# Kernel optimization log

Hardware: AMD Instinct MI355X
Metric: run time of the kernel (lower is better)

Reference implementation:

```python
import jax, jax.numpy as jnp
import numpy as np

T, B, D = 1024, 4, 1024  # seq_len, batch, d_model (module is seq-first: data[T,B,D])


def setup_inputs() -> dict:
    key = jax.random.key(0)
    ks = jax.random.split(key, 5)
    data = jax.random.normal(ks[0], (T, B, D), jnp.float32)
    # torch Linear equivalent: y = x @ W + b with W stored [in, out]
    W_qkv = jax.random.normal(ks[1], (D, 3 * D), jnp.float32) * 0.02
    b_qkv = jnp.zeros((3 * D,), jnp.float32)
    # Pos_bias param interpolated to [T,T]; with T == seq_len it's the raw param.
    pos_bias = jax.random.normal(ks[2], (T, T), jnp.float32) * 0.02
    W_out = jax.random.normal(ks[3], (D, D), jnp.float32) * 0.02
    b_out = jnp.zeros((D,), jnp.float32)
    return dict(data=data, W_qkv=W_qkv, b_qkv=b_qkv, pos_bias=pos_bias,
                W_out=W_out, b_out=b_out)


def reference(data, W_qkv, b_qkv, pos_bias, W_out, b_out):
    # layer_norm=False -> Identity; dropout unused in forward
    qkv = data @ W_qkv + b_qkv                 # [T,B,3D]
    q, k, v = jnp.split(qkv, 3, axis=-1)       # each [T,B,D]
    P = jnp.exp(pos_bias)                      # [T,T], exp of (identity-interpolated) pos bias
    ek = jnp.exp(k)                            # [T,B,D]
    # einsum 'ijb,jbd->ibd' with b==1 broadcast on pos_bias == 'tj,jbd->tbd'
    num = jnp.einsum('tj,jbd->tbd', P, ek * v)  # [T,B,D]
    den = jnp.einsum('tj,jbd->tbd', P, ek)      # [T,B,D]
    out = jax.nn.sigmoid(q) * (num / den)       # gated AFT output
    return out @ W_out + b_out                  # [T,B,D]
```

## Files before the change

kernel.cpp:

```cpp
#include <hip/hip_runtime.h>
#include <hip/hip_bf16.h>
#include <cstdint>
#include <cstddef>


typedef __bf16 bf16_t;
typedef __attribute__((ext_vector_type(8))) __bf16 bf16x8;
typedef __attribute__((ext_vector_type(4))) __bf16 bf16x4;
typedef __attribute__((ext_vector_type(4))) float floatx4;

#define T_DIM 1024
#define B_DIM 4
#define D_DIM 1024
#define R_DIM (T_DIM * B_DIM)
#define N_QKV (3 * D_DIM)
#define N_ND  (2 * R_DIM)

__global__ void k_prep(const float* __restrict__ data, const float* __restrict__ pos_bias,
                       const float* __restrict__ W_qkv, const float* __restrict__ W_out,
                       bf16_t* __restrict__ data_bf, bf16_t* __restrict__ P_bf,
                       bf16_t* __restrict__ WqT, bf16_t* __restrict__ WkvTi,
                       bf16_t* __restrict__ WoutT) {
    __shared__ float s[32][33];
    const int bid = blockIdx.x, tid = threadIdx.x;
    if (bid < 5120) {
        const float* in = (bid < 4096) ? data : pos_bias;
        bf16_t* out = (bid < 4096) ? data_bf : P_bf;
        int bb = (bid < 4096) ? bid : bid - 4096;
        int do_exp = (bid >= 4096);
        int i = (bb * 256 + tid) * 4;
        float4 v = *reinterpret_cast<const float4*>(in + i);
        bf16x4 o;
        if (do_exp) {
            o[0] = (bf16_t)__expf(v.x); o[1] = (bf16_t)__expf(v.y);
            o[2] = (bf16_t)__expf(v.z); o[3] = (bf16_t)__expf(v.w);
        } else {
            o[0] = (bf16_t)v.x; o[1] = (bf16_t)v.y;
            o[2] = (bf16_t)v.z; o[3] = (bf16_t)v.w;
        }
        *reinterpret_cast<bf16x4*>(out + i) = o;
    } else if (bid < 8192) {
        int idx = bid - 5120;
        int n0 = (idx % 96) * 32, k0 = (idx / 96) * 32;
        int tx = tid & 31, ty = tid >> 5;
#pragma unroll
        for (int i = 0; i < 4; ++i)
            s[ty + i * 8][tx] = W_qkv[(size_t)(k0 + ty + i * 8) * N_QKV + n0 + tx];
        __syncthreads();
#pragma unroll
        for (int i = 0; i < 4; ++i) {
            int n = n0 + ty + i * 8;
            bf16_t val = (bf16_t)s[tx][ty + i * 8];
            bf16_t* dst; size_t row;
            if (n < 1024)      { dst = WqT;   row = n; }
            else if (n < 2048) { int d = n - 1024; dst = WkvTi; row = ((d >> 4) << 5) + (d & 15); }
            else               { int d = n - 2048; dst = WkvTi; row = ((d >> 4) << 5) + (d & 15) + 16; }
            dst[row * D_DIM + k0 + tx] = val;
        }
    } else {
        int idx = bid - 8192;
        int n0 = (idx % 32) * 32, k0 = (idx / 32) * 32;
        int tx = tid & 31, ty = tid >> 5;
#pragma unroll
        for (int i = 0; i < 4; ++i)
            s[ty + i * 8][tx] = W_out[(size_t)(k0 + ty + i * 8) * D_DIM + n0 + tx];
        __syncthreads();
#pragma unroll
        for (int i = 0; i < 4; ++i)
            WoutT[(size_t)(n0 + ty + i * 8) * D_DIM + k0 + tx] = (bf16_t)s[tx][ty + i * 8];
    }
}

__device__ __forceinline__ void gload16(const bf16_t* src, bf16_t* dst) {
    __builtin_amdgcn_global_load_lds(
        (const __attribute__((address_space(1))) void*)src,
        (__attribute__((address_space(3))) void*)dst, 16, 0, 0);
}

__device__ __forceinline__ void mfma_loop(
    const bf16_t* __restrict__ aSrc0, const bf16_t* __restrict__ aSrc1,
    const bf16_t* __restrict__ bSrc0, const bf16_t* __restrict__ bSrc1,
    bf16_t* As, bf16_t* Bs, int wid, int lane, int K, floatx4 (&acc)[4][4]) {
    const int lr = lane & 15, kq = (lane >> 4) * 8;
    const int wm = wid >> 1, wn = wid & 1;
    for (int kt = 0; kt < K; kt += 32) {
        __syncthreads();
        gload16(aSrc0 + kt, As + wid * 1024);
        gload16(aSrc1 + kt, As + wid * 1024 + 512);
        gload16(bSrc0 + kt, Bs + wid * 1024);
        gload16(bSrc1 + kt, Bs + wid * 1024 + 512);
        __syncthreads();
        bf16x8 af[4], bfr[4];
#pragma unroll
        for (int m = 0; m < 4; ++m)
            af[m] = *reinterpret_cast<const bf16x8*>(As + (wm * 64 + m * 16 + lr) * 32 + kq);
#pragma unroll
        for (int n = 0; n < 4; ++n)
            bfr[n] = *reinterpret_cast<const bf16x8*>(Bs + (wn * 64 + n * 16 + lr) * 32 + kq);
#pragma unroll
        for (int m = 0; m < 4; ++m)
#pragma unroll
            for (int n = 0; n < 4; ++n)
                acc[m][n] = __builtin_amdgcn_mfma_f32_16x16x32_bf16(af[m], bfr[n], acc[m][n], 0, 0, 0);
    }
}

#define GEMM_PREAMBLE(K)                                              \
    __shared__ __align__(16) bf16_t As[128 * 32];                     \
    __shared__ __align__(16) bf16_t Bs[128 * 32];                     \
    const int tid = threadIdx.x;                                      \
    const int wid = tid >> 6, lane = tid & 63;                        \
    const int wm = wid >> 1, wn = wid & 1;                            \
    floatx4 acc[4][4];                                                \
    _Pragma("unroll") for (int m = 0; m < 4; ++m)                     \
        _Pragma("unroll") for (int n = 0; n < 4; ++n)                 \
            acc[m][n] = (floatx4){0.f, 0.f, 0.f, 0.f};                \
    const int lr = lane & 15;                                         \
    const int e0 = wid * 1024 + lane * 8;                             \
    const int ra0 = e0 >> 5, kk0 = e0 & 31;                           \
    const int ra1 = (e0 + 512) >> 5, kk1 = (e0 + 512) & 31;           \
    const int lg = lane >> 4; (void)lg; (void)K;

__global__ __launch_bounds__(256)
void k_gemm(const bf16_t* __restrict__ A, const bf16_t* __restrict__ BT,
            const float* __restrict__ bias, float* __restrict__ C,
            int M, int N, int K) {
    GEMM_PREAMBLE(K)
    const int row0 = blockIdx.x * 128, col0 = blockIdx.y * 128;
    mfma_loop(A + (size_t)(row0 + ra0) * K + kk0, A + (size_t)(row0 + ra1) * K + kk1,
              BT + (size_t)(col0 + ra0) * K + kk0, BT + (size_t)(col0 + ra1) * K + kk1,
              As, Bs, wid, lane, K, acc);
#pragma unroll
    for (int n = 0; n < 4; ++n) {
        int col = col0 + wn * 64 + n * 16 + lr;
        float bv = bias ? bias[col] : 0.0f;
#pragma unroll
        for (int m = 0; m < 4; ++m) {
            int row = row0 + wm * 64 + m * 16 + lg * 4;
            float* Cp = C + (size_t)row * N + col;
#pragma unroll
            for (int j = 0; j < 4; ++j) Cp[(size_t)j * N] = acc[m][n][j] + bv;
        }
    }
}

__global__ __launch_bounds__(256)
void k_gemm_qkv(const bf16_t* __restrict__ data_bf, const bf16_t* __restrict__ WqT,
                const bf16_t* __restrict__ WkvTi, const float* __restrict__ b_qkv,
                float* __restrict__ q_buf, bf16_t* __restrict__ BndT) {
    const int K = D_DIM;
    GEMM_PREAMBLE(K)
    const int bid = blockIdx.x;
    if (bid < 256) {
        const int row0 = (bid >> 3) * 128, col0 = (bid & 7) * 128;
        mfma_loop(data_bf + (size_t)(row0 + ra0) * K + kk0,
                  data_bf + (size_t)(row0 + ra1) * K + kk1,
                  WqT + (size_t)(col0 + ra0) * K + kk0,
                  WqT + (size_t)(col0 + ra1) * K + kk1,
                  As, Bs, wid, lane, K, acc);
#pragma unroll
        for (int n = 0; n < 4; ++n) {
            int col = col0 + wn * 64 + n * 16 + lr;
            float bv = b_qkv[col];
#pragma unroll
            for (int m = 0; m < 4; ++m) {
                int row = row0 + wm * 64 + m * 16 + lg * 4;
                float* Cp = q_buf + (size_t)row * D_DIM + col;
#pragma unroll
                for (int j = 0; j < 4; ++j) Cp[(size_t)j * D_DIM] = acc[m][n][j] + bv;
            }
        }
    } else {
        const int idx = bid - 256;
        const int b = idx >> 7;
        const int row0 = ((idx & 127) >> 3) * 128;
        const int col0 = (idx & 7) * 128;
        mfma_loop(WkvTi + (size_t)(row0 + ra0) * K + kk0,
                  WkvTi + (size_t)(row0 + ra1) * K + kk1,
                  data_bf + ((size_t)(col0 + ra0) * 4 + b) * D_DIM + kk0,
                  data_bf + ((size_t)(col0 + ra1) * 4 + b) * D_DIM + kk1,
                  As, Bs, wid, lane, K, acc);
#pragma unroll
        for (int p = 0; p < 2; ++p) {
#pragma unroll
            for (int j = 0; j < 4; ++j) {
                int gk = row0 + wm * 64 + p * 32 + lg * 4 + j;
                int d = ((gk >> 5) << 4) + (lg * 4 + j);
                float bk = b_qkv[D_DIM + d];
                float bv = b_qkv[2 * D_DIM + d];
                int r = b * D_DIM + d;
                int rr = ((r >> 4) << 5) + (r & 15);
#pragma unroll
                for (int n = 0; n < 4; ++n) {
                    int t = col0 + wn * 64 + n * 16 + lr;
                    float e = __expf(acc[2 * p][n][j] + bk);
                    float vv = acc[2 * p + 1][n][j] + bv;
                    BndT[(size_t)rr * T_DIM + t] = (bf16_t)(e * vv);
                    BndT[(size_t)(rr + 16) * T_DIM + t] = (bf16_t)e;
                }
            }
        }
    }
}

__global__ __launch_bounds__(256)
void k_gemm_aft(const bf16_t* __restrict__ A, const bf16_t* __restrict__ BT,
                const float* __restrict__ q, bf16_t* __restrict__ Y) {
    const int K = T_DIM;
    GEMM_PREAMBLE(K)
    const int row0 = blockIdx.x * 128, col0 = blockIdx.y * 128;
    mfma_loop(A + (size_t)(row0 + ra0) * K + kk0, A + (size_t)(row0 + ra1) * K + kk1,
              BT + (size_t)(col0 + ra0) * K + kk0, BT + (size_t)(col0 + ra1) * K + kk1,
              As, Bs, wid, lane, K, acc);
#pragma unroll
    for (int p = 0; p < 2; ++p) {
        int ncol = col0 + wn * 64 + p * 32 + lr;
        int r = ((ncol >> 5) << 4) + lr;
#pragma unroll
        for (int m = 0; m < 4; ++m) {
            int trow = row0 + wm * 64 + m * 16 + lg * 4;
#pragma unroll
            for (int j = 0; j < 4; ++j) {
                int t = trow + j;
                float num = acc[m][2 * p][j];
                float den = acc[m][2 * p + 1][j];
                float qv = q[(size_t)t * R_DIM + r];
                float y = num / (den * (1.0f + __expf(-qv)));
                Y[(size_t)t * R_DIM + r] = (bf16_t)y;
            }
        }
    }
}

extern "C" void kernel_launch(void* const* d_in, const int* in_sizes, int n_in,
                              void* d_out, int out_size, void* d_ws, size_t ws_size,
                              hipStream_t stream) {
    const float* data     = (const float*)d_in[0];
    const float* W_qkv    = (const float*)d_in[1];
    const float* b_qkv    = (const float*)d_in[2];
    const float* pos_bias = (const float*)d_in[3];
    const float* W_out    = (const float*)d_in[4];
    const float* b_out    = (const float*)d_in[5];
    float* out = (float*)d_out;

    char* ws = (char*)d_ws;
    const size_t MB = 1024 * 1024;
    bf16_t* data_bf = (bf16_t*)(ws + 0);
    bf16_t* WqT     = (bf16_t*)(ws + 8 * MB);
    bf16_t* WkvTi   = (bf16_t*)(ws + 10 * MB);
    bf16_t* WoutT   = (bf16_t*)(ws + 14 * MB);
    bf16_t* P_bf    = (bf16_t*)(ws + 16 * MB);
    float*  q_buf   = (float*) (ws + 18 * MB);
    bf16_t* BndT    = (bf16_t*)(ws + 34 * MB);
    bf16_t* Y       = (bf16_t*)(ws + 0);

    k_prep<<<dim3(9216), dim3(256), 0, stream>>>(data, pos_bias, W_qkv, W_out,
                                                 data_bf, P_bf, WqT, WkvTi, WoutT);
    k_gemm_qkv<<<dim3(768), dim3(256), 0, stream>>>(data_bf, WqT, WkvTi, b_qkv,
                                                    q_buf, BndT);
    k_gemm_aft<<<dim3(T_DIM / 128, N_ND / 128), dim3(256), 0, stream>>>(
        P_bf, BndT, q_buf, Y);
    k_gemm<<<dim3(R_DIM / 128, D_DIM / 128), dim3(256), 0, stream>>>(
        Y, WoutT, b_out, out, R_DIM, D_DIM, D_DIM);
}
```

Before: 178.2 us.

## Use 256x256 double-buffered tiles for QKV and AFT GEMMs

Replaces the 128x128 single-buffered QKV and AFT GEMM kernels with 256x256 tile kernels. Each uses 512 threads in 8 waves with an 8x4 MFMA fragment block per wave, and double-buffers LDS so the next K-slice loads while the current one computes. MFMA sections are wrapped in s_setprio. The larger tiles raise operand reuse and cut barrier stalls, but shrink the grids to 192 and 128 blocks, which may underfill the 256 CUs, and raise register pressure.

```diff
diff --git a/kernel.cpp b/kernel.cpp
--- a/kernel.cpp
+++ b/kernel.cpp
@@ -77,6 +77,146 @@
         (__attribute__((address_space(3))) void*)dst, 16, 0, 0);
 }
 
+__device__ __forceinline__ void stage32(const bf16_t* A0, int sA,
+                                        const bf16_t* B0, int sB, int k0,
+                                        bf16_t* AsB, bf16_t* BsB, int wid, int lane) {
+    const int r0 = wid * 16 + (lane >> 2);
+    const int c = (lane & 3) * 8;
+#pragma unroll
+    for (int j = 0; j < 2; ++j) {
+        gload16(A0 + (size_t)(r0 + j * 128) * sA + k0 + c, AsB + j * 4096 + wid * 512);
+        gload16(B0 + (size_t)(r0 + j * 128) * sB + k0 + c, BsB + j * 4096 + wid * 512);
+    }
+}
+
+__device__ __forceinline__ void tile32(const bf16_t* As, const bf16_t* Bs,
+                                       int wm, int wn, int lane, floatx4 (&acc)[8][4]) {
+    const int lr = lane & 15, k0 = (lane >> 4) * 8;
+    bf16x8 a[8], b[4];
+#pragma unroll
+    for (int mf = 0; mf < 8; ++mf)
+        a[mf] = *reinterpret_cast<const bf16x8*>(As + (wm * 128 + mf * 16 + lr) * 32 + k0);
+#pragma unroll
+    for (int nf = 0; nf < 4; ++nf)
+        b[nf] = *reinterpret_cast<const bf16x8*>(Bs + (wn * 64 + nf * 16 + lr) * 32 + k0);
+    __builtin_amdgcn_s_setprio(1);
+#pragma unroll
+    for (int mf = 0; mf < 8; ++mf)
+#pragma unroll
+        for (int nf = 0; nf < 4; ++nf)
+            acc[mf][nf] = __builtin_amdgcn_mfma_f32_16x16x32_bf16(a[mf], b[nf], acc[mf][nf], 0, 0, 0);
+    __builtin_amdgcn_s_setprio(0);
+}
+
+#define PRE256()                                                      \
+    __shared__ __align__(16) bf16_t As0[256 * 32], Bs0[256 * 32];     \
+    __shared__ __align__(16) bf16_t As1[256 * 32], Bs1[256 * 32];     \
+    const int tid = threadIdx.x;                                      \
+    const int wid = tid >> 6, lane = tid & 63;                        \
+    const int wm = wid >> 2, wn = wid & 3;                            \
+    const int lr = lane & 15, lg = lane >> 4;                         \
+    floatx4 acc[8][4];                                                \
+    _Pragma("unroll") for (int mf = 0; mf < 8; ++mf)                  \
+        _Pragma("unroll") for (int nf = 0; nf < 4; ++nf)              \
+            acc[mf][nf] = (floatx4){0.f, 0.f, 0.f, 0.f};
+
+#define LOOP256(Ab, sA, Bb, sB)                                       \
+    stage32(Ab, sA, Bb, sB, 0, As0, Bs0, wid, lane);                  \
+    __syncthreads();                                                  \
+    for (int t2 = 0; t2 < 16; ++t2) {                                 \
+        stage32(Ab, sA, Bb, sB, t2 * 64 + 32, As1, Bs1, wid, lane);   \
+        tile32(As0, Bs0, wm, wn, lane, acc);                          \
+        __syncthreads();                                              \
+        if (t2 < 15)                                                  \
+            stage32(Ab, sA, Bb, sB, t2 * 64 + 64, As0, Bs0, wid, lane);\
+        tile32(As1, Bs1, wm, wn, lane, acc);                          \
+        __syncthreads();                                              \
+    }
+
+__global__ __launch_bounds__(512, 1)
+void k_qkv256(const bf16_t* __restrict__ data_bf, const bf16_t* __restrict__ WqT,
+              const bf16_t* __restrict__ WkvTi, const float* __restrict__ b_qkv,
+              float* __restrict__ q_buf, bf16_t* __restrict__ BndT) {
+    PRE256()
+    const int bid = blockIdx.x;
+    if (bid < 64) {
+        const int row0 = (bid >> 2) * 256, col0 = (bid & 3) * 256;
+        const bf16_t* Ab = data_bf + (size_t)row0 * D_DIM;
+        const bf16_t* Bb = WqT + (size_t)col0 * D_DIM;
+        LOOP256(Ab, D_DIM, Bb, D_DIM)
+#pragma unroll
+        for (int nf = 0; nf < 4; ++nf) {
+            int col = col0 + wn * 64 + nf * 16 + lr;
+            float bv = b_qkv[col];
+#pragma unroll
+            for (int mf = 0; mf < 8; ++mf) {
+                int row = row0 + wm * 128 + mf * 16 + lg * 4;
+                float* Cp = q_buf + (size_t)row * D_DIM + col;
+#pragma unroll
+                for (int j = 0; j < 4; ++j) Cp[(size_t)j * D_DIM] = acc[mf][nf][j] + bv;
+            }
+        }
+    } else {
+        const int idx = bid - 64;
+        const int b = idx >> 5;
+        const int row0 = ((idx & 31) >> 2) * 256;
+        const int col0 = (idx & 3) * 256;
+        const bf16_t* Ab = WkvTi + (size_t)row0 * D_DIM;
+        const bf16_t* Bb = data_bf + ((size_t)col0 * 4 + b) * D_DIM;
+        LOOP256(Ab, D_DIM, Bb, 4 * D_DIM)
+#pragma unroll
+        for (int p = 0; p < 4; ++p) {
+#pragma unroll
+            for (int j = 0; j < 4; ++j) {
+                int gk = row0 + wm * 128 + p * 32 + lg * 4 + j;
+                int d = ((gk >> 5) << 4) + (lg * 4 + j);
+                float bk = b_qkv[D_DIM + d];
+                float bvv = b_qkv[2 * D_DIM + d];
+                int r = b * D_DIM + d;
+                int rr = ((r >> 4) << 5) + (r & 15);
+#pragma unroll
+                for (int nf = 0; nf < 4; ++nf) {
+                    int t = col0 + wn * 64 + nf * 16 + lr;
+                    float e = __expf(acc[2 * p][nf][j] + bk);
+                    float vv = acc[2 * p + 1][nf][j] + bvv;
+                    BndT[(size_t)rr * T_DIM + t] = (bf16_t)(e * vv);
+                    BndT[(size_t)(rr + 16) * T_DIM + t] = (bf16_t)e;
+                }
+            }
+        }
+    }
+}
+
+__global__ __launch_bounds__(512, 1)
+void k_aft256(const bf16_t* __restrict__ P_bf, const bf16_t* __restrict__ BndT,
+              const float* __restrict__ q, bf16_t* __restrict__ Y) {
+    PRE256()
+    const int bid = blockIdx.x;
+    const int row0 = (bid >> 5) * 256;
+    const int col0 = (bid & 31) * 256;
+    const bf16_t* Ab = P_bf + (size_t)row0 * T_DIM;
+    const bf16_t* Bb = BndT + (size_t)col0 * T_DIM;
+    LOOP256(Ab, T_DIM, Bb, T_DIM)
+#pragma unroll
+    for (int p = 0; p < 2; ++p) {
+        int ncol = col0 + wn * 64 + p * 32 + lr;
+        int r = ((ncol >> 5) << 4) + lr;
+#pragma unroll
+        for (int mf = 0; mf < 8; ++mf) {
+            int trow = row0 + wm * 128 + mf * 16 + lg * 4;
+#pragma unroll
+            for (int j = 0; j < 4; ++j) {
+                int t = trow + j;
+                float num = acc[mf][2 * p][j];
+                float den = acc[mf][2 * p + 1][j];
+                float qv = q[(size_t)t * R_DIM + r];
+                float y = num / (den * (1.0f + __expf(-qv)));
+                Y[(size_t)t * R_DIM + r] = (bf16_t)y;
+            }
+        }
+    }
+}
+
 __device__ __forceinline__ void mfma_loop(
     const bf16_t* __restrict__ aSrc0, const bf16_t* __restrict__ aSrc1,
     const bf16_t* __restrict__ bSrc0, const bf16_t* __restrict__ bSrc1,
@@ -105,27 +245,25 @@
     }
 }
 
-#define GEMM_PREAMBLE(K)                                              \
-    __shared__ __align__(16) bf16_t As[128 * 32];                     \
-    __shared__ __align__(16) bf16_t Bs[128 * 32];                     \
-    const int tid = threadIdx.x;                                      \
-    const int wid = tid >> 6, lane = tid & 63;                        \
-    const int wm = wid >> 1, wn = wid & 1;                            \
-    floatx4 acc[4][4];                                                \
-    _Pragma("unroll") for (int m = 0; m < 4; ++m)                     \
-        _Pragma("unroll") for (int n = 0; n < 4; ++n)                 \
-            acc[m][n] = (floatx4){0.f, 0.f, 0.f, 0.f};                \
-    const int lr = lane & 15;                                         \
-    const int e0 = wid * 1024 + lane * 8;                             \
-    const int ra0 = e0 >> 5, kk0 = e0 & 31;                           \
-    const int ra1 = (e0 + 512) >> 5, kk1 = (e0 + 512) & 31;           \
-    const int lg = lane >> 4; (void)lg; (void)K;
-
 __global__ __launch_bounds__(256)
 void k_gemm(const bf16_t* __restrict__ A, const bf16_t* __restrict__ BT,
             const float* __restrict__ bias, float* __restrict__ C,
             int M, int N, int K) {
-    GEMM_PREAMBLE(K)
+    __shared__ __align__(16) bf16_t As[128 * 32];
+    __shared__ __align__(16) bf16_t Bs[128 * 32];
+    const int tid = threadIdx.x;
+    const int wid = tid >> 6, lane = tid & 63;
+    const int wm = wid >> 1, wn = wid & 1;
+    floatx4 acc[4][4];
+#pragma unroll
+    for (int m = 0; m < 4; ++m)
+#pragma unroll
+        for (int n = 0; n < 4; ++n) acc[m][n] = (floatx4){0.f, 0.f, 0.f, 0.f};
+    const int lr = lane & 15;
+    const int e0 = wid * 1024 + lane * 8;
+    const int ra0 = e0 >> 5, kk0 = e0 & 31;
+    const int ra1 = (e0 + 512) >> 5, kk1 = (e0 + 512) & 31;
+    const int lg = lane >> 4;
     const int row0 = blockIdx.x * 128, col0 = blockIdx.y * 128;
     mfma_loop(A + (size_t)(row0 + ra0) * K + kk0, A + (size_t)(row0 + ra1) * K + kk1,
               BT + (size_t)(col0 + ra0) * K + kk0, BT + (size_t)(col0 + ra1) * K + kk1,
@@ -140,94 +278,6 @@
             float* Cp = C + (size_t)row * N + col;
 #pragma unroll
             for (int j = 0; j < 4; ++j) Cp[(size_t)j * N] = acc[m][n][j] + bv;
-        }
-    }
-}
-
-__global__ __launch_bounds__(256)
-void k_gemm_qkv(const bf16_t* __restrict__ data_bf, const bf16_t* __restrict__ WqT,
-                const bf16_t* __restrict__ WkvTi, const float* __restrict__ b_qkv,
-                float* __restrict__ q_buf, bf16_t* __restrict__ BndT) {
-    const int K = D_DIM;
-    GEMM_PREAMBLE(K)
-    const int bid = blockIdx.x;
-    if (bid < 256) {
-        const int row0 = (bid >> 3) * 128, col0 = (bid & 7) * 128;
-        mfma_loop(data_bf + (size_t)(row0 + ra0) * K + kk0,
-                  data_bf + (size_t)(row0 + ra1) * K + kk1,
-                  WqT + (size_t)(col0 + ra0) * K + kk0,
-                  WqT + (size_t)(col0 + ra1) * K + kk1,
-                  As, Bs, wid, lane, K, acc);
-#pragma unroll
-        for (int n = 0; n < 4; ++n) {
-            int col = col0 + wn * 64 + n * 16 + lr;
-            float bv = b_qkv[col];
-#pragma unroll
-            for (int m = 0; m < 4; ++m) {
-                int row = row0 + wm * 64 + m * 16 + lg * 4;
-                float* Cp = q_buf + (size_t)row * D_DIM + col;
-#pragma unroll
-                for (int j = 0; j < 4; ++j) Cp[(size_t)j * D_DIM] = acc[m][n][j] + bv;
-            }
-        }
-    } else {
-        const int idx = bid - 256;
-        const int b = idx >> 7;
-        const int row0 = ((idx & 127) >> 3) * 128;
-        const int col0 = (idx & 7) * 128;
-        mfma_loop(WkvTi + (size_t)(row0 + ra0) * K + kk0,
-                  WkvTi + (size_t)(row0 + ra1) * K + kk1,
-                  data_bf + ((size_t)(col0 + ra0) * 4 + b) * D_DIM + kk0,
-                  data_bf + ((size_t)(col0 + ra1) * 4 + b) * D_DIM + kk1,
-                  As, Bs, wid, lane, K, acc);
-#pragma unroll
-        for (int p = 0; p < 2; ++p) {
-#pragma unroll
-            for (int j = 0; j < 4; ++j) {
-                int gk = row0 + wm * 64 + p * 32 + lg * 4 + j;
-                int d = ((gk >> 5) << 4) + (lg * 4 + j);
-                float bk = b_qkv[D_DIM + d];
-                float bv = b_qkv[2 * D_DIM + d];
-                int r = b * D_DIM + d;
-                int rr = ((r >> 4) << 5) + (r & 15);
-#pragma unroll
-                for (int n = 0; n < 4; ++n) {
-                    int t = col0 + wn * 64 + n * 16 + lr;
-                    float e = __expf(acc[2 * p][n][j] + bk);
-                    float vv = acc[2 * p + 1][n][j] + bv;
-                    BndT[(size_t)rr * T_DIM + t] = (bf16_t)(e * vv);
-                    BndT[(size_t)(rr + 16) * T_DIM + t] = (bf16_t)e;
-                }
-            }
-        }
-    }
-}
-
-__global__ __launch_bounds__(256)
-void k_gemm_aft(const bf16_t* __restrict__ A, const bf16_t* __restrict__ BT,
-                const float* __restrict__ q, bf16_t* __restrict__ Y) {
-    const int K = T_DIM;
-    GEMM_PREAMBLE(K)
-    const int row0 = blockIdx.x * 128, col0 = blockIdx.y * 128;
-    mfma_loop(A + (size_t)(row0 + ra0) * K + kk0, A + (size_t)(row0 + ra1) * K + kk1,
-              BT + (size_t)(col0 + ra0) * K + kk0, BT + (size_t)(col0 + ra1) * K + kk1,
-              As, Bs, wid, lane, K, acc);
-#pragma unroll
-    for (int p = 0; p < 2; ++p) {
-        int ncol = col0 + wn * 64 + p * 32 + lr;
-        int r = ((ncol >> 5) << 4) + lr;
-#pragma unroll
-        for (int m = 0; m < 4; ++m) {
-            int trow = row0 + wm * 64 + m * 16 + lg * 4;
-#pragma unroll
-            for (int j = 0; j < 4; ++j) {
-                int t = trow + j;
-                float num = acc[m][2 * p][j];
-                float den = acc[m][2 * p + 1][j];
-                float qv = q[(size_t)t * R_DIM + r];
-                float y = num / (den * (1.0f + __expf(-qv)));
-                Y[(size_t)t * R_DIM + r] = (bf16_t)y;
-            }
         }
     }
 }
@@ -256,10 +306,9 @@
 
     k_prep<<<dim3(9216), dim3(256), 0, stream>>>(data, pos_bias, W_qkv, W_out,
                                                  data_bf, P_bf, WqT, WkvTi, WoutT);
-    k_gemm_qkv<<<dim3(768), dim3(256), 0, stream>>>(data_bf, WqT, WkvTi, b_qkv,
-                                                    q_buf, BndT);
-    k_gemm_aft<<<dim3(T_DIM / 128, N_ND / 128), dim3(256), 0, stream>>>(
-        P_bf, BndT, q_buf, Y);
+    k_qkv256<<<dim3(192), dim3(512), 0, stream>>>(data_bf, WqT, WkvTi, b_qkv,
+                                                  q_buf, BndT);
+    k_aft256<<<dim3(128), dim3(512), 0, stream>>>(P_bf, BndT, q_buf, Y);
     k_gemm<<<dim3(R_DIM / 128, D_DIM / 128), dim3(256), 0, stream>>>(
         Y, WoutT, b_out, out, R_DIM, D_DIM, D_DIM);
 }
```

Result: slower. 183.2 us (+2.8%).
